# Performance work log

Measured on AMD Instinct MI355X. Metric: run time of the kernel, lower is better.

## Reference

```python
import jax, jax.numpy as jnp
import numpy as np

V, E, H, F, B = 32000, 1024, 1024, 2048, 64
NL = 8  # number of GRU cells


def _gru_cell(x, h, Wih, Whh, bih, bhh):
    # PyTorch GRU single-step math. x:[B,E], h:[B,H], Wih:[3H,E], Whh:[3H,H]
    gi = x @ Wih.T + bih            # [B,3H]
    gh = h @ Whh.T + bhh            # [B,3H]
    i_r, i_z, i_n = jnp.split(gi, 3, axis=1)
    h_r, h_z, h_n = jnp.split(gh, 3, axis=1)
    r = jax.nn.sigmoid(i_r + h_r)
    z = jax.nn.sigmoid(i_z + h_z)
    n = jnp.tanh(i_n + r * h_n)
    return (1.0 - z) * n + z * h


def setup_inputs() -> dict:
    key = jax.random.key(0)
    ks = jax.random.split(key, 20)
    s = 0.02
    inp = {
        "feature": jax.random.normal(ks[0], (B, F), jnp.float32),
        "x": jax.random.randint(ks[1], (B,), 0, V),
        "attention": jax.random.normal(ks[2], (B, H), jnp.float32),
        "hiddens": jax.random.normal(ks[3], (NL, B, H), jnp.float32),
        "emb": jax.random.normal(ks[4], (V, E), jnp.float32) * s,
        "map_W": jax.random.normal(ks[5], (H, F), jnp.float32) * s,
        "map_b": jnp.zeros((H,), jnp.float32),
        "ai_W": jax.random.normal(ks[6], (H, H), jnp.float32) * s,
        "ai_b": jnp.zeros((H,), jnp.float32),
        "ah_W": jax.random.normal(ks[7], (H, H), jnp.float32) * s,
        "ah_b": jnp.zeros((H,), jnp.float32),
        "ao_W": jax.random.normal(ks[8], (H, H), jnp.float32) * s,
        "ao_b": jnp.zeros((H,), jnp.float32),
        "gru_Wih": jax.random.normal(ks[9], (NL, 3 * H, E), jnp.float32) * s,
        "gru_Whh": jax.random.normal(ks[10], (NL, 3 * H, H), jnp.float32) * s,
        "gru_bih": jnp.zeros((NL, 3 * H), jnp.float32),
        "gru_bhh": jnp.zeros((NL, 3 * H), jnp.float32),
        "out_W": jax.random.normal(ks[11], (V, H), jnp.float32) * s,
        "out_b": jnp.zeros((V,), jnp.float32),
    }
    return inp


def reference(feature, x, attention, hiddens, emb, map_W, map_b, ai_W, ai_b,
              ah_W, ah_b, ao_W, ao_b, gru_Wih, gru_Whh, gru_bih, gru_bhh,
              out_W, out_b):
    xe = jax.nn.relu(emb[x])                                  # [B,E]
    feat = jax.nn.relu(feature @ map_W.T + map_b)             # [B,H]
    attn = jax.nn.relu((feat + attention) @ ai_W.T + ai_b)
    attn = jax.nn.relu(attn @ ah_W.T + ah_b)
    attn = jax.nn.relu(attn @ ao_W.T + ao_b)                  # [B,H]

    def cell(i, xin):
        return _gru_cell(xin, hiddens[i] + attn, gru_Wih[i], gru_Whh[i],
                         gru_bih[i], gru_bhh[i])

    h1 = cell(0, xe)          # new attention output
    x2 = cell(1, h1)
    x3 = cell(2, x2)
    x4 = cell(3, x2 + x3)
    x5 = cell(4, x3 + x4)
    x6 = cell(5, x4 + x5)
    x7 = cell(6, x5 + x6)
    x8 = cell(7, x6 + x7)

    logp = jax.nn.log_softmax(x8 @ out_W.T + out_b, axis=1)   # [B,V]
    new_hiddens = jnp.stack([h1, x2, x3, x4, x5, x6, x7, x8])  # [8,B,H]
    return (logp, h1, new_hiddens)
```

## Files before the change

### kernel.cpp

```cpp
#include <hip/hip_runtime.h>
#include <math.h>

typedef __bf16 bf16x8 __attribute__((ext_vector_type(8)));
typedef float f32x4 __attribute__((ext_vector_type(4)));

__device__ __forceinline__ __bf16 f2bf(float f) {
    union { float f; unsigned u; } v; v.f = f;
    unsigned r = v.u + 0x7FFF + ((v.u >> 16) & 1);
    union { unsigned short s; __bf16 b; } c; c.s = (unsigned short)(r >> 16);
    return c.b;
}

template <int RELU>
__device__ __forceinline__ bf16x8 ld8(const float* p) {
    f32x4 lo = *reinterpret_cast<const f32x4*>(p);
    f32x4 hi = *reinterpret_cast<const f32x4*>(p + 4);
    bf16x8 r;
#pragma unroll
    for (int i = 0; i < 4; ++i) {
        float a = lo[i], b = hi[i];
        if (RELU) { a = fmaxf(a, 0.0f); b = fmaxf(b, 0.0f); }
        r[i] = f2bf(a); r[i + 4] = f2bf(b);
    }
    return r;
}

__device__ __forceinline__ bf16x8 ld8ra(const float* p, const float* rp) {
    f32x4 lo = *reinterpret_cast<const f32x4*>(p);
    f32x4 hi = *reinterpret_cast<const f32x4*>(p + 4);
    f32x4 rl = *reinterpret_cast<const f32x4*>(rp);
    f32x4 rh = *reinterpret_cast<const f32x4*>(rp + 4);
    bf16x8 r;
#pragma unroll
    for (int i = 0; i < 4; ++i) {
        r[i]     = f2bf(fmaxf(lo[i], 0.0f) + rl[i]);
        r[i + 4] = f2bf(fmaxf(hi[i], 0.0f) + rh[i]);
    }
    return r;
}

__device__ __forceinline__ void atomAdd(float* p, float v) {
#if __has_builtin(__builtin_amdgcn_global_atomic_fadd_f32)
    unsafeAtomicAdd(p, v);
#else
    atomicAdd(p, v);
#endif
}

template <int MODE_A>
__global__ __launch_bounds__(64) void gemm_acc(
    const float* __restrict__ A, long long Asb,
    const float* __restrict__ W, long long Wsb,
    const float* __restrict__ Ares,
    float* __restrict__ out, long long osb,
    int K, int KC, int N)
{
    const int l = threadIdx.x;
    const int lane16 = l & 15;
    const int quad = l >> 4;
    const int layer = blockIdx.z;
    const int n = blockIdx.x * 16 + lane16;
    const int k0 = blockIdx.y * KC;

    A += (long long)layer * Asb + k0 + quad * 8;
    W += (long long)layer * Wsb + k0 + quad * 8;
    if (MODE_A == 2) Ares += k0 + quad * 8;

    const float* wp  = W + (long long)n * K;
    const float* ap0 = A + (long long)(lane16 + 0) * K;
    const float* ap1 = A + (long long)(lane16 + 16) * K;
    const float* ap2 = A + (long long)(lane16 + 32) * K;
    const float* ap3 = A + (long long)(lane16 + 48) * K;
    const float* rp0 = Ares + (long long)(lane16 + 0) * K;
    const float* rp1 = Ares + (long long)(lane16 + 16) * K;
    const float* rp2 = Ares + (long long)(lane16 + 32) * K;
    const float* rp3 = Ares + (long long)(lane16 + 48) * K;

    f32x4 acc0 = {0.f, 0.f, 0.f, 0.f};
    f32x4 acc1 = acc0, acc2 = acc0, acc3 = acc0;

#pragma unroll 4
    for (int k = 0; k < KC; k += 32) {
        bf16x8 b = ld8<0>(wp + k);
        bf16x8 a0, a1, a2, a3;
        if (MODE_A == 2) {
            a0 = ld8ra(ap0 + k, rp0 + k);
            a1 = ld8ra(ap1 + k, rp1 + k);
            a2 = ld8ra(ap2 + k, rp2 + k);
            a3 = ld8ra(ap3 + k, rp3 + k);
        } else {
            a0 = ld8<MODE_A>(ap0 + k);
            a1 = ld8<MODE_A>(ap1 + k);
            a2 = ld8<MODE_A>(ap2 + k);
            a3 = ld8<MODE_A>(ap3 + k);
        }
        acc0 = __builtin_amdgcn_mfma_f32_16x16x32_bf16(a0, b, acc0, 0, 0, 0);
        acc1 = __builtin_amdgcn_mfma_f32_16x16x32_bf16(a1, b, acc1, 0, 0, 0);
        acc2 = __builtin_amdgcn_mfma_f32_16x16x32_bf16(a2, b, acc2, 0, 0, 0);
        acc3 = __builtin_amdgcn_mfma_f32_16x16x32_bf16(a3, b, acc3, 0, 0, 0);
    }

    f32x4 accs[4] = {acc0, acc1, acc2, acc3};
    float* ob = out + (long long)layer * osb + n;
#pragma unroll
    for (int mt = 0; mt < 4; ++mt)
#pragma unroll
        for (int r = 0; r < 4; ++r) {
            const int m = mt * 16 + quad * 4 + r;
            atomAdd(ob + (long long)m * N, accs[mt][r]);
        }
}

__global__ __launch_bounds__(256) void init_acc(
    const float* __restrict__ map_b,
    const float* __restrict__ ai_b, const float* __restrict__ ah_b,
    const float* __restrict__ ao_b, const float* __restrict__ gru_bhh,
    const float* __restrict__ gru_bih, const float* __restrict__ out_b,
    float* __restrict__ t0, float* __restrict__ a1b, float* __restrict__ a2b,
    float* __restrict__ attnb, float* __restrict__ gh, float* __restrict__ gi,
    float* __restrict__ logp)
{
    int idx = blockIdx.x * 256 + threadIdx.x;
    if (idx < 65536) { t0[idx] = map_b[idx & 1023]; return; }
    idx -= 65536;
    if (idx < 65536) { a1b[idx] = ai_b[idx & 1023]; return; }
    idx -= 65536;
    if (idx < 65536) { a2b[idx] = ah_b[idx & 1023]; return; }
    idx -= 65536;
    if (idx < 65536) { attnb[idx] = ao_b[idx & 1023]; return; }
    idx -= 65536;
    if (idx < 1572864) {
        const int layer = idx / 196608, col = idx % 3072;
        gh[idx] = gru_bhh[layer * 3072 + col];
        return;
    }
    idx -= 1572864;
    if (idx < 1572864) {
        const int layer = idx / 196608, col = idx % 3072;
        gi[idx] = gru_bih[layer * 3072 + col];
        return;
    }
    idx -= 1572864;
    if (idx < 2048000) logp[idx] = out_b[idx % 32000];
}

__global__ __launch_bounds__(256) void gather_relu(
    const float* __restrict__ emb, const int* __restrict__ xidx,
    float* __restrict__ xe)
{
    const int gid = blockIdx.x * 256 + threadIdx.x;
    const int m = gid >> 10, e = gid & 1023;
    xe[gid] = fmaxf(emb[(long long)xidx[m] * 1024 + e], 0.0f);
}

__global__ __launch_bounds__(256) void hsum(
    const float* __restrict__ hiddens, const float* __restrict__ attn,
    float* __restrict__ h)
{
    const int gid = blockIdx.x * 256 + threadIdx.x;
    h[gid] = hiddens[gid] + fmaxf(attn[gid & 65535], 0.0f);
}

__global__ __launch_bounds__(256) void gru_pw(
    const float* __restrict__ gi, const float* __restrict__ gh,
    const float* __restrict__ h, const float* __restrict__ oprev,
    float* __restrict__ o_out, float* __restrict__ o_out2,
    float* __restrict__ xin_next)
{
    const int gid = blockIdx.x * 256 + threadIdx.x;
    const int m = gid >> 10, nn = gid & 1023;
    const long long gb = (long long)m * 3072 + nn;
    const float i_r = gi[gb], i_z = gi[gb + 1024], i_n = gi[gb + 2048];
    const float h_r = gh[gb], h_z = gh[gb + 1024], h_n = gh[gb + 2048];
    const float r = 1.0f / (1.0f + __expf(-(i_r + h_r)));
    const float z = 1.0f / (1.0f + __expf(-(i_z + h_z)));
    const float nv = tanhf(i_n + r * h_n);
    const float x = (1.0f - z) * nv + z * h[gid];
    o_out[gid] = x;
    if (o_out2) o_out2[gid] = x;
    float xi = x;
    if (oprev) xi += oprev[gid];
    xin_next[gid] = xi;
}

__global__ __launch_bounds__(256) void rowstats(
    const float* __restrict__ logits, float* __restrict__ stats)
{
    const int m = blockIdx.x;
    const f32x4* row = reinterpret_cast<const f32x4*>(logits + (long long)m * 32000);
    __shared__ float red[256];
    const int tid = threadIdx.x;
    float mx = -1e30f;
    for (int i = tid; i < 8000; i += 256) {
        f32x4 v = row[i];
        mx = fmaxf(mx, fmaxf(fmaxf(v[0], v[1]), fmaxf(v[2], v[3])));
    }
    red[tid] = mx;
    __syncthreads();
    for (int off = 128; off > 0; off >>= 1) {
        if (tid < off) red[tid] = fmaxf(red[tid], red[tid + off]);
        __syncthreads();
    }
    mx = red[0];
    __syncthreads();
    float s = 0.0f;
    for (int i = tid; i < 8000; i += 256) {
        f32x4 v = row[i];
        s += __expf(v[0] - mx) + __expf(v[1] - mx) + __expf(v[2] - mx) + __expf(v[3] - mx);
    }
    red[tid] = s;
    __syncthreads();
    for (int off = 128; off > 0; off >>= 1) {
        if (tid < off) red[tid] += red[tid + off];
        __syncthreads();
    }
    if (tid == 0) stats[m] = mx + logf(red[0]);
}

__global__ __launch_bounds__(256) void logp_k(
    float* __restrict__ out, const float* __restrict__ stats)
{
    const int n = blockIdx.x * 256 + threadIdx.x;
    const int m = blockIdx.y;
    const long long idx = (long long)m * 32000 + n;
    out[idx] = out[idx] - stats[m];
}

extern "C" void kernel_launch(void* const* d_in, const int* in_sizes, int n_in,
                              void* d_out, int out_size, void* d_ws, size_t ws_size,
                              hipStream_t stream)
{
    const float* feature   = (const float*)d_in[0];
    const int*   x         = (const int*)d_in[1];
    const float* attention = (const float*)d_in[2];
    const float* hiddens   = (const float*)d_in[3];
    const float* emb       = (const float*)d_in[4];
    const float* map_W     = (const float*)d_in[5];
    const float* map_b     = (const float*)d_in[6];
    const float* ai_W      = (const float*)d_in[7];
    const float* ai_b      = (const float*)d_in[8];
    const float* ah_W      = (const float*)d_in[9];
    const float* ah_b      = (const float*)d_in[10];
    const float* ao_W      = (const float*)d_in[11];
    const float* ao_b      = (const float*)d_in[12];
    const float* gru_Wih   = (const float*)d_in[13];
    const float* gru_Whh   = (const float*)d_in[14];
    const float* gru_bih   = (const float*)d_in[15];
    const float* gru_bhh   = (const float*)d_in[16];
    const float* out_W     = (const float*)d_in[17];
    const float* out_b     = (const float*)d_in[18];

    float* out      = (float*)d_out;
    float* out_logp = out;
    float* out_h1   = out + 2048000;
    float* out_nh   = out + 2048000 + 65536;

    float* w = (float*)d_ws;
    float* xin   = w + 0;
    float* t0    = w + 65536;
    float* a1b   = w + 131072;
    float* a2b   = w + 196608;
    float* attnb = w + 262144;
    float* hbuf  = w + 327680;
    float* gh    = w + 851968;
    float* gi    = w + 2424832;
    float* stats = w + 3997696;

    init_acc<<<21312, 256, 0, stream>>>(map_b, ai_b, ah_b, ao_b,
                                        gru_bhh, gru_bih, out_b,
                                        t0, a1b, a2b, attnb, gh, gi, out_logp);
    gather_relu<<<256, 256, 0, stream>>>(emb, x, xin);

    gemm_acc<0><<<dim3(64, 16, 1), 64, 0, stream>>>(feature, 0, map_W, 0, nullptr,
                                                    t0, 0, 2048, 128, 1024);
    gemm_acc<2><<<dim3(64, 8, 1), 64, 0, stream>>>(t0, 0, ai_W, 0, attention,
                                                   a1b, 0, 1024, 128, 1024);
    gemm_acc<1><<<dim3(64, 8, 1), 64, 0, stream>>>(a1b, 0, ah_W, 0, nullptr,
                                                   a2b, 0, 1024, 128, 1024);
    gemm_acc<1><<<dim3(64, 8, 1), 64, 0, stream>>>(a2b, 0, ao_W, 0, nullptr,
                                                   attnb, 0, 1024, 128, 1024);

    hsum<<<2048, 256, 0, stream>>>(hiddens, attnb, hbuf);

    gemm_acc<0><<<dim3(192, 2, 8), 64, 0, stream>>>(hbuf, 65536, gru_Whh, 3145728,
                                                    nullptr, gh, 196608,
                                                    1024, 512, 3072);

    for (int c = 0; c < 8; ++c) {
        gemm_acc<0><<<dim3(192, 8, 1), 64, 0, stream>>>(
            xin, 0, gru_Wih + (long long)c * 3145728, 0, nullptr,
            gi + (long long)c * 196608, 0, 1024, 128, 3072);
        gru_pw<<<256, 256, 0, stream>>>(
            gi + (long long)c * 196608, gh + (long long)c * 196608,
            hbuf + (long long)c * 65536,
            (c >= 2) ? out_nh + (long long)(c - 1) * 65536 : nullptr,
            out_nh + (long long)c * 65536,
            (c == 0) ? out_h1 : nullptr,
            xin);
    }

    gemm_acc<0><<<dim3(2000, 2, 1), 64, 0, stream>>>(out_nh + 7LL * 65536, 0,
                                                     out_W, 0, nullptr,
                                                     out_logp, 0, 1024, 512, 32000);

    rowstats<<<64, 256, 0, stream>>>(out_logp, stats);
    logp_k<<<dim3(125, 64), 256, 0, stream>>>(out_logp, stats);
}
```

Baseline: 698.3 us.

## Pre-convert GEMM activations to bf16 and pack four waves per block

Result: faster. 596.1 us (-14.6%).

```diff
diff --git a/kernel.cpp b/kernel.cpp
--- a/kernel.cpp
+++ b/kernel.cpp
@@ -2,42 +2,8 @@
 #include <math.h>
 
 typedef __bf16 bf16x8 __attribute__((ext_vector_type(8)));
+typedef __bf16 bf16x4 __attribute__((ext_vector_type(4)));
 typedef float f32x4 __attribute__((ext_vector_type(4)));
-
-__device__ __forceinline__ __bf16 f2bf(float f) {
-    union { float f; unsigned u; } v; v.f = f;
-    unsigned r = v.u + 0x7FFF + ((v.u >> 16) & 1);
-    union { unsigned short s; __bf16 b; } c; c.s = (unsigned short)(r >> 16);
-    return c.b;
-}
-
-template <int RELU>
-__device__ __forceinline__ bf16x8 ld8(const float* p) {
-    f32x4 lo = *reinterpret_cast<const f32x4*>(p);
-    f32x4 hi = *reinterpret_cast<const f32x4*>(p + 4);
-    bf16x8 r;
-#pragma unroll
-    for (int i = 0; i < 4; ++i) {
-        float a = lo[i], b = hi[i];
-        if (RELU) { a = fmaxf(a, 0.0f); b = fmaxf(b, 0.0f); }
-        r[i] = f2bf(a); r[i + 4] = f2bf(b);
-    }
-    return r;
-}
-
-__device__ __forceinline__ bf16x8 ld8ra(const float* p, const float* rp) {
-    f32x4 lo = *reinterpret_cast<const f32x4*>(p);
-    f32x4 hi = *reinterpret_cast<const f32x4*>(p + 4);
-    f32x4 rl = *reinterpret_cast<const f32x4*>(rp);
-    f32x4 rh = *reinterpret_cast<const f32x4*>(rp + 4);
-    bf16x8 r;
-#pragma unroll
-    for (int i = 0; i < 4; ++i) {
-        r[i]     = f2bf(fmaxf(lo[i], 0.0f) + rl[i]);
-        r[i + 4] = f2bf(fmaxf(hi[i], 0.0f) + rh[i]);
-    }
-    return r;
-}
 
 __device__ __forceinline__ void atomAdd(float* p, float v) {
 #if __has_builtin(__builtin_amdgcn_global_atomic_fadd_f32)
@@ -47,53 +13,46 @@
 #endif
 }
 
-template <int MODE_A>
-__global__ __launch_bounds__(64) void gemm_acc(
-    const float* __restrict__ A, long long Asb,
+__device__ __forceinline__ bf16x8 cvt8(const float* p) {
+    f32x4 lo = *reinterpret_cast<const f32x4*>(p);
+    f32x4 hi = *reinterpret_cast<const f32x4*>(p + 4);
+    bf16x8 r;
+#pragma unroll
+    for (int i = 0; i < 4; ++i) { r[i] = (__bf16)lo[i]; r[i + 4] = (__bf16)hi[i]; }
+    return r;
+}
+
+__global__ __launch_bounds__(256) void gemm_acc(
+    const __bf16* __restrict__ A, long long Asb,
     const float* __restrict__ W, long long Wsb,
-    const float* __restrict__ Ares,
     float* __restrict__ out, long long osb,
     int K, int KC, int N)
 {
-    const int l = threadIdx.x;
+    const int l = threadIdx.x & 63;
+    const int wave = threadIdx.x >> 6;
     const int lane16 = l & 15;
     const int quad = l >> 4;
     const int layer = blockIdx.z;
-    const int n = blockIdx.x * 16 + lane16;
+    const int n = (blockIdx.x * 4 + wave) * 16 + lane16;
     const int k0 = blockIdx.y * KC;
 
     A += (long long)layer * Asb + k0 + quad * 8;
-    W += (long long)layer * Wsb + k0 + quad * 8;
-    if (MODE_A == 2) Ares += k0 + quad * 8;
-
-    const float* wp  = W + (long long)n * K;
-    const float* ap0 = A + (long long)(lane16 + 0) * K;
-    const float* ap1 = A + (long long)(lane16 + 16) * K;
-    const float* ap2 = A + (long long)(lane16 + 32) * K;
-    const float* ap3 = A + (long long)(lane16 + 48) * K;
-    const float* rp0 = Ares + (long long)(lane16 + 0) * K;
-    const float* rp1 = Ares + (long long)(lane16 + 16) * K;
-    const float* rp2 = Ares + (long long)(lane16 + 32) * K;
-    const float* rp3 = Ares + (long long)(lane16 + 48) * K;
+    const float* wp = W + (long long)layer * Wsb + (long long)n * K + k0 + quad * 8;
+    const __bf16* ap0 = A + (long long)(lane16 +  0) * K;
+    const __bf16* ap1 = A + (long long)(lane16 + 16) * K;
+    const __bf16* ap2 = A + (long long)(lane16 + 32) * K;
+    const __bf16* ap3 = A + (long long)(lane16 + 48) * K;
 
     f32x4 acc0 = {0.f, 0.f, 0.f, 0.f};
     f32x4 acc1 = acc0, acc2 = acc0, acc3 = acc0;
 
 #pragma unroll 4
     for (int k = 0; k < KC; k += 32) {
-        bf16x8 b = ld8<0>(wp + k);
-        bf16x8 a0, a1, a2, a3;
-        if (MODE_A == 2) {
-            a0 = ld8ra(ap0 + k, rp0 + k);
-            a1 = ld8ra(ap1 + k, rp1 + k);
-            a2 = ld8ra(ap2 + k, rp2 + k);
-            a3 = ld8ra(ap3 + k, rp3 + k);
-        } else {
-            a0 = ld8<MODE_A>(ap0 + k);
-            a1 = ld8<MODE_A>(ap1 + k);
-            a2 = ld8<MODE_A>(ap2 + k);
-            a3 = ld8<MODE_A>(ap3 + k);
-        }
+        bf16x8 b  = cvt8(wp + k);
+        bf16x8 a0 = *reinterpret_cast<const bf16x8*>(ap0 + k);
+        bf16x8 a1 = *reinterpret_cast<const bf16x8*>(ap1 + k);
+        bf16x8 a2 = *reinterpret_cast<const bf16x8*>(ap2 + k);
+        bf16x8 a3 = *reinterpret_cast<const bf16x8*>(ap3 + k);
         acc0 = __builtin_amdgcn_mfma_f32_16x16x32_bf16(a0, b, acc0, 0, 0, 0);
         acc1 = __builtin_amdgcn_mfma_f32_16x16x32_bf16(a1, b, acc1, 0, 0, 0);
         acc2 = __builtin_amdgcn_mfma_f32_16x16x32_bf16(a2, b, acc2, 0, 0, 0);
@@ -109,6 +68,27 @@
             const int m = mt * 16 + quad * 4 + r;
             atomAdd(ob + (long long)m * N, accs[mt][r]);
         }
+}
+
+template <int RELU, int RES>
+__global__ __launch_bounds__(256) void conv_bf(
+    const float* __restrict__ in, const float* __restrict__ res,
+    __bf16* __restrict__ out, int total4)
+{
+    const int gid = blockIdx.x * 256 + threadIdx.x;
+    if (gid >= total4) return;
+    f32x4 v = reinterpret_cast<const f32x4*>(in)[gid];
+    f32x4 rv;
+    if (RES) rv = reinterpret_cast<const f32x4*>(res)[gid];
+    bf16x4 o;
+#pragma unroll
+    for (int i = 0; i < 4; ++i) {
+        float a = v[i];
+        if (RELU) a = fmaxf(a, 0.0f);
+        if (RES) a += rv[i];
+        o[i] = (__bf16)a;
+    }
+    reinterpret_cast<bf16x4*>(out)[gid] = o;
 }
 
 __global__ __launch_bounds__(256) void init_acc(
@@ -146,26 +126,36 @@
 
 __global__ __launch_bounds__(256) void gather_relu(
     const float* __restrict__ emb, const int* __restrict__ xidx,
-    float* __restrict__ xe)
+    __bf16* __restrict__ xe)
 {
     const int gid = blockIdx.x * 256 + threadIdx.x;
-    const int m = gid >> 10, e = gid & 1023;
-    xe[gid] = fmaxf(emb[(long long)xidx[m] * 1024 + e], 0.0f);
+    const int m = gid >> 8, e = (gid & 255) << 2;
+    f32x4 v = *reinterpret_cast<const f32x4*>(emb + (long long)xidx[m] * 1024 + e);
+    bf16x4 o;
+#pragma unroll
+    for (int i = 0; i < 4; ++i) o[i] = (__bf16)fmaxf(v[i], 0.0f);
+    *reinterpret_cast<bf16x4*>(xe + ((long long)m << 10) + e) = o;
 }
 
 __global__ __launch_bounds__(256) void hsum(
     const float* __restrict__ hiddens, const float* __restrict__ attn,
-    float* __restrict__ h)
+    __bf16* __restrict__ hbf)
 {
     const int gid = blockIdx.x * 256 + threadIdx.x;
-    h[gid] = hiddens[gid] + fmaxf(attn[gid & 65535], 0.0f);
+    f32x4 hv = reinterpret_cast<const f32x4*>(hiddens)[gid];
+    f32x4 av = reinterpret_cast<const f32x4*>(attn)[gid & 16383];
+    bf16x4 o;
+#pragma unroll
+    for (int i = 0; i < 4; ++i) o[i] = (__bf16)(hv[i] + fmaxf(av[i], 0.0f));
+    reinterpret_cast<bf16x4*>(hbf)[gid] = o;
 }
 
 __global__ __launch_bounds__(256) void gru_pw(
     const float* __restrict__ gi, const float* __restrict__ gh,
-    const float* __restrict__ h, const float* __restrict__ oprev,
+    const float* __restrict__ hiddens, const float* __restrict__ attn,
+    const float* __restrict__ oprev,
     float* __restrict__ o_out, float* __restrict__ o_out2,
-    float* __restrict__ xin_next)
+    __bf16* __restrict__ xin_next)
 {
     const int gid = blockIdx.x * 256 + threadIdx.x;
     const int m = gid >> 10, nn = gid & 1023;
@@ -175,12 +165,13 @@
     const float r = 1.0f / (1.0f + __expf(-(i_r + h_r)));
     const float z = 1.0f / (1.0f + __expf(-(i_z + h_z)));
     const float nv = tanhf(i_n + r * h_n);
-    const float x = (1.0f - z) * nv + z * h[gid];
+    const float hcur = hiddens[gid] + fmaxf(attn[gid], 0.0f);
+    const float x = (1.0f - z) * nv + z * hcur;
     o_out[gid] = x;
     if (o_out2) o_out2[gid] = x;
     float xi = x;
     if (oprev) xi += oprev[gid];
-    xin_next[gid] = xi;
+    xin_next[gid] = (__bf16)xi;
 }
 
 __global__ __launch_bounds__(256) void rowstats(
@@ -256,52 +247,58 @@
     float* out_nh   = out + 2048000 + 65536;
 
     float* w = (float*)d_ws;
-    float* xin   = w + 0;
-    float* t0    = w + 65536;
-    float* a1b   = w + 131072;
-    float* a2b   = w + 196608;
-    float* attnb = w + 262144;
-    float* hbuf  = w + 327680;
-    float* gh    = w + 851968;
-    float* gi    = w + 2424832;
-    float* stats = w + 3997696;
+    float* t0    = w + 0;
+    float* a1b   = w + 65536;
+    float* a2b   = w + 131072;
+    float* attnb = w + 196608;
+    float* gh    = w + 262144;
+    float* gi    = w + 1835008;
+    float* stats = w + 3407872;
+    __bf16* xin   = (__bf16*)(w + 3407936);
+    __bf16* featb = (__bf16*)(w + 3440704);
+    __bf16* a1A   = (__bf16*)(w + 3506240);
+    __bf16* a2A   = (__bf16*)(w + 3539008);
+    __bf16* a3A   = (__bf16*)(w + 3571776);
+    __bf16* hbf   = (__bf16*)(w + 3604544);
 
     init_acc<<<21312, 256, 0, stream>>>(map_b, ai_b, ah_b, ao_b,
                                         gru_bhh, gru_bih, out_b,
                                         t0, a1b, a2b, attnb, gh, gi, out_logp);
-    gather_relu<<<256, 256, 0, stream>>>(emb, x, xin);
-
-    gemm_acc<0><<<dim3(64, 16, 1), 64, 0, stream>>>(feature, 0, map_W, 0, nullptr,
-                                                    t0, 0, 2048, 128, 1024);
-    gemm_acc<2><<<dim3(64, 8, 1), 64, 0, stream>>>(t0, 0, ai_W, 0, attention,
-                                                   a1b, 0, 1024, 128, 1024);
-    gemm_acc<1><<<dim3(64, 8, 1), 64, 0, stream>>>(a1b, 0, ah_W, 0, nullptr,
-                                                   a2b, 0, 1024, 128, 1024);
-    gemm_acc<1><<<dim3(64, 8, 1), 64, 0, stream>>>(a2b, 0, ao_W, 0, nullptr,
-                                                   attnb, 0, 1024, 128, 1024);
-
-    hsum<<<2048, 256, 0, stream>>>(hiddens, attnb, hbuf);
-
-    gemm_acc<0><<<dim3(192, 2, 8), 64, 0, stream>>>(hbuf, 65536, gru_Whh, 3145728,
-                                                    nullptr, gh, 196608,
-                                                    1024, 512, 3072);
+    gather_relu<<<64, 256, 0, stream>>>(emb, x, xin);
+    conv_bf<0, 0><<<128, 256, 0, stream>>>(feature, nullptr, featb, 32768);
+
+    gemm_acc<<<dim3(16, 16, 1), 256, 0, stream>>>(featb, 0, map_W, 0,
+                                                  t0, 0, 2048, 128, 1024);
+    conv_bf<1, 1><<<64, 256, 0, stream>>>(t0, attention, a1A, 16384);
+    gemm_acc<<<dim3(16, 8, 1), 256, 0, stream>>>(a1A, 0, ai_W, 0,
+                                                 a1b, 0, 1024, 128, 1024);
+    conv_bf<1, 0><<<64, 256, 0, stream>>>(a1b, nullptr, a2A, 16384);
+    gemm_acc<<<dim3(16, 8, 1), 256, 0, stream>>>(a2A, 0, ah_W, 0,
+                                                 a2b, 0, 1024, 128, 1024);
+    conv_bf<1, 0><<<64, 256, 0, stream>>>(a2b, nullptr, a3A, 16384);
+    gemm_acc<<<dim3(16, 8, 1), 256, 0, stream>>>(a3A, 0, ao_W, 0,
+                                                 attnb, 0, 1024, 128, 1024);
+
+    hsum<<<512, 256, 0, stream>>>(hiddens, attnb, hbf);
+
+    gemm_acc<<<dim3(48, 2, 8), 256, 0, stream>>>(hbf, 65536, gru_Whh, 3145728,
+                                                 gh, 196608, 1024, 512, 3072);
 
     for (int c = 0; c < 8; ++c) {
-        gemm_acc<0><<<dim3(192, 8, 1), 64, 0, stream>>>(
-            xin, 0, gru_Wih + (long long)c * 3145728, 0, nullptr,
+        gemm_acc<<<dim3(48, 8, 1), 256, 0, stream>>>(
+            xin, 0, gru_Wih + (long long)c * 3145728, 0,
             gi + (long long)c * 196608, 0, 1024, 128, 3072);
         gru_pw<<<256, 256, 0, stream>>>(
             gi + (long long)c * 196608, gh + (long long)c * 196608,
-            hbuf + (long long)c * 65536,
-            (c >= 2) ? out_nh + (long long)(c - 1) * 65536 : nullptr,
+            hiddens + (long long)c * 65536, attnb,
+            (c >= 2 && c < 7) ? out_nh + (long long)(c - 1) * 65536 : nullptr,
             out_nh + (long long)c * 65536,
             (c == 0) ? out_h1 : nullptr,
             xin);
     }
 
-    gemm_acc<0><<<dim3(2000, 2, 1), 64, 0, stream>>>(out_nh + 7LL * 65536, 0,
-                                                     out_W, 0, nullptr,
-                                                     out_logp, 0, 1024, 512, 32000);
+    gemm_acc<<<dim3(500, 2, 1), 256, 0, stream>>>(xin, 0, out_W, 0,
+                                                  out_logp, 0, 1024, 512, 32000);
 
     rowstats<<<64, 256, 0, stream>>>(out_logp, stats);
     logp_k<<<dim3(125, 64), 256, 0, stream>>>(out_logp, stats);
```
